# Kernel optimization log

Measured on AMD Instinct MI355X. Metric: run time of the kernel, lower is better.

Reference implementation:

```python
import jax, jax.numpy as jnp
import numpy as np

L_SEQ = 32768
H_FEAT = 512
P_STATE = 256  # state_size // 2 (conj_sym)
LOG_DT_MIN, LOG_DT_MAX = np.log(1e-3), np.log(1e-1)


def setup_inputs() -> dict:
    key = jax.random.key(0)
    ks = jax.random.split(key, 7)
    input_sequence = jax.random.normal(ks[0], (L_SEQ, H_FEAT), dtype=jnp.float32)
    # eigenvalue real parts must be negative for stability (HiPPO-LegS-like)
    lambda_real = -jax.random.uniform(ks[1], (P_STATE,), minval=0.1, maxval=1.0, dtype=jnp.float32)
    lambda_imag = jax.random.normal(ks[2], (P_STATE,), dtype=jnp.float32) * float(np.pi)
    b = jax.random.normal(ks[3], (P_STATE, H_FEAT, 2), dtype=jnp.float32) / np.sqrt(H_FEAT)
    c = jax.random.normal(ks[4], (H_FEAT, P_STATE, 2), dtype=jnp.float32) / np.sqrt(P_STATE)
    d = jax.random.normal(ks[5], (H_FEAT,), dtype=jnp.float32)
    # log-timestep init in [log(1e-3), log(1e-1)] as in init_log_steps
    delta = (LOG_DT_MIN + jax.random.uniform(ks[6], (P_STATE, 1), dtype=jnp.float32)
             * (LOG_DT_MAX - LOG_DT_MIN))
    return {"input_sequence": input_sequence, "lambda_real": lambda_real,
            "lambda_imag": lambda_imag, "b": b, "c": c, "d": d, "delta": delta}


def _binop(e_i, e_j):
    A_i, b_i = e_i
    A_j, b_j = e_j
    return A_j * A_i, A_j * b_i + b_j


def reference(input_sequence, lambda_real, lambda_imag, b, c, d, delta):
    # assemble complex parameters (stored as real [..., 2])
    Lam = lambda_real + 1j * lambda_imag            # [P]
    B = b[..., 0] + 1j * b[..., 1]                  # [P, H]
    C = c[..., 0] + 1j * c[..., 1]                  # [H, P]
    step = jnp.exp(delta[:, 0])                     # step_rescale = 1.0
    # bilinear discretization
    BL = 1.0 / (1.0 - (step / 2.0) * Lam)
    Lam_bar = BL * (1.0 + (step / 2.0) * Lam)       # [P]
    B_bar = (BL * step)[:, None] * B                # [P, H]
    # input projection: Bu[l] = B_bar @ u[l]
    Bu = jnp.einsum('lh,ph->lp', input_sequence.astype(Lam_bar.dtype), B_bar)  # [L, P]
    L = input_sequence.shape[0]
    Lam_el = jnp.broadcast_to(Lam_bar, (L, Lam_bar.shape[0]))
    _, xs = jax.lax.associative_scan(_binop, (Lam_el, Bu))  # xs: [L, P] complex states
    # output projection (conj_sym => factor 2, real part)
    ys = 2.0 * jnp.einsum('lp,hp->lh', xs, C).real  # [L, H]
    return ys + d * input_sequence
```

## Files before the change

### kernel.cpp

```cpp
#include <hip/hip_runtime.h>
#include <cstddef>

#define L_SEQ 32768
#define H_FEAT 512
#define P_STATE 256
#define N2 512
#define CS 32
#define NCH (L_SEQ / CS)

typedef __bf16 bf16x8 __attribute__((ext_vector_type(8)));
typedef float f32x4 __attribute__((ext_vector_type(4)));

#define GLDS16(g, l) __builtin_amdgcn_global_load_lds( \
    (const __attribute__((address_space(1))) void*)(g), \
    (__attribute__((address_space(3))) void*)(l), 16, 0, 0)

__device__ __forceinline__ unsigned bf_rne(float x) {
    unsigned u = __float_as_uint(x);
    return (u + 0x7fffu + ((u >> 16) & 1u)) >> 16;
}
__device__ __forceinline__ float bf_f(unsigned bits) {
    return __uint_as_float(bits << 16);
}

__global__ __launch_bounds__(256) void param_kernel(
    const float* __restrict__ lr, const float* __restrict__ li,
    const float* __restrict__ b,  const float* __restrict__ c,
    const float* __restrict__ delta,
    ushort* __restrict__ W_hi, ushort* __restrict__ W_lo,
    ushort* __restrict__ C2_hi, ushort* __restrict__ C2_lo,
    float2* __restrict__ Abar)
{
    int tid = blockIdx.x * blockDim.x + threadIdx.x;

    {
        int p = tid >> 9;
        int h = tid & 511;
        float step = expf(delta[p]);
        float zr = 0.5f * step * lr[p];
        float zi = 0.5f * step * li[p];
        float dr = 1.0f - zr, di = -zi;
        float den = dr * dr + di * di;
        float blr = dr / den, bli = -di / den;
        float bbr = blr * step, bbi = bli * step;
        float b0 = b[((size_t)(p * H_FEAT + h)) * 2 + 0];
        float b1 = b[((size_t)(p * H_FEAT + h)) * 2 + 1];
        float vr = bbr * b0 - bbi * b1;
        float vi = bbr * b1 + bbi * b0;
        unsigned hr = bf_rne(vr), hl = bf_rne(vr - bf_f(hr));
        unsigned ir = bf_rne(vi), il = bf_rne(vi - bf_f(ir));
        size_t o0 = (size_t)(2 * p) * H_FEAT + h;
        size_t o1 = (size_t)(2 * p + 1) * H_FEAT + h;
        W_hi[o0] = (ushort)hr; W_lo[o0] = (ushort)hl;
        W_hi[o1] = (ushort)ir; W_lo[o1] = (ushort)il;
    }

    {
        int h2 = tid >> 8;
        int p2 = tid & 255;
        float c0 =  2.0f * c[((size_t)(h2 * P_STATE + p2)) * 2 + 0];
        float c1 = -2.0f * c[((size_t)(h2 * P_STATE + p2)) * 2 + 1];
        unsigned h0 = bf_rne(c0), l0 = bf_rne(c0 - bf_f(h0));
        unsigned h1 = bf_rne(c1), l1 = bf_rne(c1 - bf_f(h1));
        size_t o0 = (size_t)h2 * N2 + 2 * p2;
        C2_hi[o0] = (ushort)h0;     C2_lo[o0] = (ushort)l0;
        C2_hi[o0 + 1] = (ushort)h1; C2_lo[o0 + 1] = (ushort)l1;
    }

    if (tid < P_STATE) {
        int p = tid;
        float step = expf(delta[p]);
        float zr = 0.5f * step * lr[p];
        float zi = 0.5f * step * li[p];
        float dr = 1.0f - zr, di = -zi;
        float den = dr * dr + di * di;
        float blr = dr / den, bli = -di / den;
        float nr = 1.0f + zr, ni = zi;
        Abar[p] = make_float2(blr * nr - bli * ni, blr * ni + bli * nr);
    }
}

__global__ __launch_bounds__(256, 2) void gemm1(
    const float* __restrict__ A,
    const ushort* __restrict__ Bhi, const ushort* __restrict__ Blo,
    float* __restrict__ C,
    const float2* __restrict__ Abar, float2* __restrict__ ends)
{
    __shared__ ushort sh[24576];
    ushort* As_hi = sh;
    ushort* As_lo = sh + 4096;
    ushort* Bs_hi = sh + 8192;
    ushort* Bs_lo = sh + 16384;
    float*  Cs    = (float*)(sh + 8192);

    const int tid = threadIdx.x;
    const int ln = tid & 63, wv = tid >> 6;
    const int bm = blockIdx.y * 128, bn = blockIdx.x * 256;
    const int m = ln & 15, q = ln >> 4;
    const int wr = (wv >> 1) * 64, wc = (wv & 1) * 128;

    f32x4 acc[4][8] = {};

    for (int k0 = 0; k0 < 512; k0 += 32) {
#pragma unroll
        for (int s = 0; s < 8; s++) {
            int t = wv * 8 + s;
            int ch = t & 15;
            int row = ch * 16 + (ln >> 2);
            const ushort* src = (t < 16 ? Bhi : Blo)
                                + (size_t)(bn + row) * 512 + k0 + (ln & 3) * 8;
            ushort* dst = (t < 16 ? Bs_hi : Bs_lo) + ch * 512 + ln * 8;
            GLDS16(src, dst);
        }
#pragma unroll
        for (int r = 0; r < 4; r++) {
            int idx = tid + r * 256;
            int row = idx >> 3;
            int c4 = (idx & 7) << 2;
            const float4 v = *(const float4*)(A + (size_t)(bm + row) * 512 + k0 + c4);
            unsigned u0 = __float_as_uint(v.x), u1 = __float_as_uint(v.y);
            unsigned u2 = __float_as_uint(v.z), u3 = __float_as_uint(v.w);
            unsigned hi01 = (u0 >> 16) | (u1 & 0xffff0000u);
            unsigned hi23 = (u2 >> 16) | (u3 & 0xffff0000u);
            float d0 = v.x - __uint_as_float(u0 & 0xffff0000u);
            float d1 = v.y - __uint_as_float(u1 & 0xffff0000u);
            float d2 = v.z - __uint_as_float(u2 & 0xffff0000u);
            float d3 = v.w - __uint_as_float(u3 & 0xffff0000u);
            unsigned lo01 = (__float_as_uint(d0) >> 16) | (__float_as_uint(d1) & 0xffff0000u);
            unsigned lo23 = (__float_as_uint(d2) >> 16) | (__float_as_uint(d3) & 0xffff0000u);
            *(uint2*)(As_hi + row * 32 + c4) = make_uint2(hi01, hi23);
            *(uint2*)(As_lo + row * 32 + c4) = make_uint2(lo01, lo23);
        }
        __syncthreads();

        bf16x8 ah[4], al[4];
#pragma unroll
        for (int i = 0; i < 4; i++) {
            ah[i] = *(const bf16x8*)(As_hi + (wr + i * 16 + m) * 32 + q * 8);
            al[i] = *(const bf16x8*)(As_lo + (wr + i * 16 + m) * 32 + q * 8);
        }
#pragma unroll
        for (int j = 0; j < 8; j++) {
            bf16x8 bh = *(const bf16x8*)(Bs_hi + (wc + j * 16 + m) * 32 + q * 8);
            bf16x8 bl = *(const bf16x8*)(Bs_lo + (wc + j * 16 + m) * 32 + q * 8);
#pragma unroll
            for (int i = 0; i < 4; i++)
                acc[i][j] = __builtin_amdgcn_mfma_f32_16x16x32_bf16(ah[i], bh, acc[i][j], 0, 0, 0);
#pragma unroll
            for (int i = 0; i < 4; i++)
                acc[i][j] = __builtin_amdgcn_mfma_f32_16x16x32_bf16(al[i], bh, acc[i][j], 0, 0, 0);
#pragma unroll
            for (int i = 0; i < 4; i++)
                acc[i][j] = __builtin_amdgcn_mfma_f32_16x16x32_bf16(ah[i], bl, acc[i][j], 0, 0, 0);
        }
        __syncthreads();
    }

#pragma unroll
    for (int i = 0; i < 4; i++)
#pragma unroll
        for (int j = 0; j < 8; j++)
#pragma unroll
            for (int r = 0; r < 4; r++) {
                int row = bm + wr + i * 16 + q * 4 + r;
                int col = bn + wc + j * 16 + m;
                C[(size_t)row * 512 + col] = acc[i][j][r];
            }

    float2 Aop;
    if (tid < 128) Aop = Abar[(bn >> 1) + tid];
#pragma unroll
    for (int c = 0; c < 4; c++) {
        if ((wv >> 1) == (c >> 1)) {
#pragma unroll
            for (int ii = 0; ii < 2; ii++) {
                int i = (c & 1) * 2 + ii;
#pragma unroll
                for (int j = 0; j < 8; j++)
#pragma unroll
                    for (int r = 0; r < 4; r++)
                        Cs[(ii * 16 + q * 4 + r) * 256 + wc + j * 16 + m] = acc[i][j][r];
            }
        }
        __syncthreads();
        if (tid < 128) {
            float2 s = make_float2(0.f, 0.f);
#pragma unroll 8
            for (int i2 = 0; i2 < 32; i2++) {
                float2 u = *(const float2*)(Cs + i2 * 256 + 2 * tid);
                float sr = fmaf(Aop.x, s.x, fmaf(-Aop.y, s.y, u.x));
                float si = fmaf(Aop.x, s.y, fmaf(Aop.y, s.x, u.y));
                s = make_float2(sr, si);
            }
            ends[(size_t)((bn >> 1) + tid) * NCH + (bm >> 5) + c] = s;
        }
        __syncthreads();
    }
}

__global__ __launch_bounds__(256, 2) void gemm2(
    const float* __restrict__ Bu,
    const ushort* __restrict__ Bhi, const ushort* __restrict__ Blo,
    float* __restrict__ Cout, const float* __restrict__ U,
    const float* __restrict__ dvec,
    const float2* __restrict__ Abar, const float2* __restrict__ carries)
{
    __shared__ ushort As_hi[128 * 32], As_lo[128 * 32];
    __shared__ ushort Bs_hi[256 * 32], Bs_lo[256 * 32];
    __shared__ float  Af32[128 * 32];
    const int tid = threadIdx.x;
    const int ln = tid & 63, wv = tid >> 6;
    const int bm = blockIdx.y * 128, bn = blockIdx.x * 256;
    const int m = ln & 15, q = ln >> 4;
    const int wr = (wv >> 1) * 64, wc = (wv & 1) * 128;

    f32x4 acc[4][8] = {};

    for (int k0 = 0; k0 < 512; k0 += 32) {
#pragma unroll
        for (int s = 0; s < 8; s++) {
            int t = wv * 8 + s;
            int ch = t & 15;
            int row = ch * 16 + (ln >> 2);
            const ushort* src = (t < 16 ? Bhi : Blo)
                                + (size_t)(bn + row) * 512 + k0 + (ln & 3) * 8;
            ushort* dst = (t < 16 ? Bs_hi : Bs_lo) + ch * 512 + ln * 8;
            GLDS16(src, dst);
        }
#pragma unroll
        for (int r = 0; r < 4; r++) {
            int idx = tid + r * 256;
            int row = idx >> 3;
            int c4 = (idx & 7) << 2;
            const float4 v = *(const float4*)(Bu + (size_t)(bm + row) * 512 + k0 + c4);
            *(float4*)(Af32 + row * 32 + c4) = v;
        }
        __syncthreads();

        if (tid < 64) {
            const int pl = tid & 15, ch = tid >> 4;
            const int pg = (k0 >> 1) + pl;
            const float2 Aop = Abar[pg];
            float2 s = carries[(size_t)pg * NCH + (bm >> 5) + ch];
#pragma unroll 8
            for (int i = 0; i < 32; i++) {
                const int row = ch * 32 + i;
                const float2 uv = *(const float2*)(Af32 + row * 32 + 2 * pl);
                float sr = fmaf(Aop.x, s.x, fmaf(-Aop.y, s.y, uv.x));
                float si = fmaf(Aop.x, s.y, fmaf(Aop.y, s.x, uv.y));
                s = make_float2(sr, si);
                unsigned hr  = bf_rne(sr);
                unsigned lr2 = __float_as_uint(sr - bf_f(hr)) >> 16;
                unsigned hi_ = bf_rne(si);
                unsigned li2 = __float_as_uint(si - bf_f(hi_)) >> 16;
                *(unsigned*)(As_hi + row * 32 + 2 * pl) = hr | (hi_ << 16);
                *(unsigned*)(As_lo + row * 32 + 2 * pl) = lr2 | (li2 << 16);
            }
        }
        __syncthreads();

        bf16x8 ah[4], al[4];
#pragma unroll
        for (int i = 0; i < 4; i++) {
            ah[i] = *(const bf16x8*)(As_hi + (wr + i * 16 + m) * 32 + q * 8);
            al[i] = *(const bf16x8*)(As_lo + (wr + i * 16 + m) * 32 + q * 8);
        }
#pragma unroll
        for (int j = 0; j < 8; j++) {
            bf16x8 bh = *(const bf16x8*)(Bs_hi + (wc + j * 16 + m) * 32 + q * 8);
            bf16x8 bl = *(const bf16x8*)(Bs_lo + (wc + j * 16 + m) * 32 + q * 8);
#pragma unroll
            for (int i = 0; i < 4; i++)
                acc[i][j] = __builtin_amdgcn_mfma_f32_16x16x32_bf16(ah[i], bh, acc[i][j], 0, 0, 0);
#pragma unroll
            for (int i = 0; i < 4; i++)
                acc[i][j] = __builtin_amdgcn_mfma_f32_16x16x32_bf16(al[i], bh, acc[i][j], 0, 0, 0);
#pragma unroll
            for (int i = 0; i < 4; i++)
                acc[i][j] = __builtin_amdgcn_mfma_f32_16x16x32_bf16(ah[i], bl, acc[i][j], 0, 0, 0);
        }
        __syncthreads();
    }

#pragma unroll
    for (int i = 0; i < 4; i++)
#pragma unroll
        for (int j = 0; j < 8; j++) {
            int col = bn + wc + j * 16 + m;
            float dv = dvec[col];
#pragma unroll
            for (int r = 0; r < 4; r++) {
                int row = bm + wr + i * 16 + q * 4 + r;
                Cout[(size_t)row * 512 + col] =
                    acc[i][j][r] + dv * U[(size_t)row * 512 + col];
            }
        }
}

__global__ __launch_bounds__(1024) void scan_pass2(
    const float2* __restrict__ ends, const float2* __restrict__ Abar,
    float2* __restrict__ carries)
{
    __shared__ float2 sA[NCH];
    __shared__ float2 sB[NCH];
    int p = blockIdx.x;
    int t = threadIdx.x;

    float2 a = Abar[p];
#pragma unroll
    for (int i = 0; i < 5; i++) {
        float nr = a.x * a.x - a.y * a.y;
        float ni = 2.f * a.x * a.y;
        a = make_float2(nr, ni);
    }
    float2 A = a;
    float2 bv = ends[(size_t)p * NCH + t];
    sA[t] = A; sB[t] = bv;
    __syncthreads();

    for (int off = 1; off < NCH; off <<= 1) {
        float2 pa, pb;
        bool act = (t >= off);
        if (act) { pa = sA[t - off]; pb = sB[t - off]; }
        __syncthreads();
        if (act) {
            float2 nA = make_float2(A.x * pa.x - A.y * pa.y,
                                    A.x * pa.y + A.y * pa.x);
            float2 nB = make_float2(fmaf(A.x, pb.x, fmaf(-A.y, pb.y, bv.x)),
                                    fmaf(A.x, pb.y, fmaf(A.y, pb.x, bv.y)));
            A = nA; bv = nB;
            sA[t] = A; sB[t] = bv;
        }
        __syncthreads();
    }

    float2 carry = (t == 0) ? make_float2(0.f, 0.f) : sB[t - 1];
    carries[(size_t)p * NCH + t] = carry;
}

extern "C" void kernel_launch(void* const* d_in, const int* in_sizes, int n_in,
                              void* d_out, int out_size, void* d_ws, size_t ws_size,
                              hipStream_t stream) {
    const float* u     = (const float*)d_in[0];
    const float* lr    = (const float*)d_in[1];
    const float* li    = (const float*)d_in[2];
    const float* b     = (const float*)d_in[3];
    const float* c     = (const float*)d_in[4];
    const float* dvec  = (const float*)d_in[5];
    const float* delta = (const float*)d_in[6];
    float* out = (float*)d_out;

    char* p = (char*)d_ws;
    float*  Bu      = (float*)p;   p += (size_t)L_SEQ * N2 * 4;
    float2* ends    = (float2*)p;  p += (size_t)P_STATE * NCH * 8;
    float2* carries = (float2*)p;  p += (size_t)P_STATE * NCH * 8;
    ushort* W_hi    = (ushort*)p;  p += (size_t)N2 * H_FEAT * 2;
    ushort* W_lo    = (ushort*)p;  p += (size_t)N2 * H_FEAT * 2;
    ushort* C2_hi   = (ushort*)p;  p += (size_t)H_FEAT * N2 * 2;
    ushort* C2_lo   = (ushort*)p;  p += (size_t)H_FEAT * N2 * 2;
    float2* Abar    = (float2*)p;  p += (size_t)P_STATE * 8;

    param_kernel<<<(P_STATE * H_FEAT) / 256, 256, 0, stream>>>(
        lr, li, b, c, delta, W_hi, W_lo, C2_hi, C2_lo, Abar);

    {
        dim3 grid(N2 / 256, L_SEQ / 128);
        gemm1<<<grid, 256, 0, stream>>>(u, W_hi, W_lo, Bu, Abar, ends);
    }

    scan_pass2<<<P_STATE, NCH, 0, stream>>>(ends, Abar, carries);

    {
        dim3 grid(H_FEAT / 256, L_SEQ / 128);
        gemm2<<<grid, 256, 0, stream>>>(Bu, C2_hi, C2_lo, out, u, dvec,
                                        Abar, carries);
    }
}
```

Baseline: 246.3 us.

## Parallelize in-GEMM chunk scan across all 256 threads with sub-chunk carry composition

```diff
diff --git a/kernel.cpp b/kernel.cpp
--- a/kernel.cpp
+++ b/kernel.cpp
@@ -21,6 +21,13 @@
 }
 __device__ __forceinline__ float bf_f(unsigned bits) {
     return __uint_as_float(bits << 16);
+}
+__device__ __forceinline__ float2 cmul(float2 a, float2 b) {
+    return make_float2(fmaf(a.x, b.x, -a.y * b.y), fmaf(a.x, b.y, a.y * b.x));
+}
+__device__ __forceinline__ float2 cfma(float2 a, float2 b, float2 c) {
+    return make_float2(fmaf(a.x, b.x, fmaf(-a.y, b.y, c.x)),
+                       fmaf(a.x, b.y, fmaf(a.y, b.x, c.y)));
 }
 
 __global__ __launch_bounds__(256) void param_kernel(
@@ -214,6 +221,8 @@
     const int m = ln & 15, q = ln >> 4;
     const int wr = (wv >> 1) * 64, wc = (wv & 1) * 128;
 
+    const int pl = tid & 15, sg = (tid >> 4) & 3, chk = tid >> 6;
+
     f32x4 acc[4][8] = {};
 
     for (int k0 = 0; k0 < 512; k0 += 32) {
@@ -237,24 +246,42 @@
         }
         __syncthreads();
 
-        if (tid < 64) {
-            const int pl = tid & 15, ch = tid >> 4;
+        {
             const int pg = (k0 >> 1) + pl;
-            const float2 Aop = Abar[pg];
-            float2 s = carries[(size_t)pg * NCH + (bm >> 5) + ch];
-#pragma unroll 8
-            for (int i = 0; i < 32; i++) {
-                const int row = ch * 32 + i;
-                const float2 uv = *(const float2*)(Af32 + row * 32 + 2 * pl);
-                float sr = fmaf(Aop.x, s.x, fmaf(-Aop.y, s.y, uv.x));
-                float si = fmaf(Aop.x, s.y, fmaf(Aop.y, s.x, uv.y));
-                s = make_float2(sr, si);
+            const float2 Aop2 = Abar[pg];
+            const float2 A2 = cmul(Aop2, Aop2);
+            const float2 A4 = cmul(A2, A2);
+            const float2 A8 = cmul(A4, A4);
+            const int rbase = chk * 32 + sg * 8;
+
+            float2 lv[8];
+            float2 s = make_float2(0.f, 0.f);
+#pragma unroll
+            for (int k = 0; k < 8; k++) {
+                const float2 uv = *(const float2*)(Af32 + (rbase + k) * 32 + 2 * pl);
+                s = cfma(Aop2, s, uv);
+                lv[k] = s;
+            }
+            const float2 e0 = make_float2(__shfl(s.x, pl),      __shfl(s.y, pl));
+            const float2 e1 = make_float2(__shfl(s.x, pl + 16), __shfl(s.y, pl + 16));
+            const float2 e2 = make_float2(__shfl(s.x, pl + 32), __shfl(s.y, pl + 32));
+            float2 S = carries[(size_t)pg * NCH + (bm >> 5) + chk];
+            if (sg >= 1) S = cfma(A8, S, e0);
+            if (sg >= 2) S = cfma(A8, S, e1);
+            if (sg >= 3) S = cfma(A8, S, e2);
+            float2 pw = Aop2;
+#pragma unroll
+            for (int k = 0; k < 8; k++) {
+                const float sr = fmaf(pw.x, S.x, fmaf(-pw.y, S.y, lv[k].x));
+                const float si = fmaf(pw.x, S.y, fmaf(pw.y, S.x, lv[k].y));
                 unsigned hr  = bf_rne(sr);
                 unsigned lr2 = __float_as_uint(sr - bf_f(hr)) >> 16;
                 unsigned hi_ = bf_rne(si);
                 unsigned li2 = __float_as_uint(si - bf_f(hi_)) >> 16;
+                const int row = rbase + k;
                 *(unsigned*)(As_hi + row * 32 + 2 * pl) = hr | (hi_ << 16);
                 *(unsigned*)(As_lo + row * 32 + 2 * pl) = lr2 | (li2 << 16);
+                pw = cmul(pw, Aop2);
             }
         }
         __syncthreads();
```

New measurement: 234.6 us. 1.05x faster.
